# Kernel optimization log

Hardware: AMD Instinct MI355X
Metric: run time of the kernel (lower is better)

The kernel has to match this reference:

```python
import jax, jax.numpy as jnp
import numpy as np

N = 100000
E = 3200000
IN_CH = 256
HID = 32
OUT_CH = 16


def setup_inputs() -> dict:
    key = jax.random.key(0)
    ks = jax.random.split(key, 9)
    x = jax.random.normal(ks[0], (N, IN_CH), dtype=jnp.float32)
    row = jax.random.randint(ks[1], (E,), 0, N)
    col = jax.random.randint(ks[2], (E,), 0, N)
    edge_index = jnp.stack([row, col], axis=0)  # [2, E]
    # Glorot-style init for GCN weights, zero bias (PyG default)
    def glorot(k, fan_in, fan_out):
        s = jnp.sqrt(6.0 / (fan_in + fan_out))
        return jax.random.uniform(k, (fan_in, fan_out), jnp.float32, -s, s)
    W1 = glorot(ks[3], IN_CH, HID)
    b1 = jnp.zeros((HID,), jnp.float32)
    W_mu = glorot(ks[4], HID, OUT_CH)
    b_mu = jnp.zeros((OUT_CH,), jnp.float32)
    W_lv = glorot(ks[5], HID, OUT_CH)
    b_lv = jnp.zeros((OUT_CH,), jnp.float32)
    return {"x": x, "edge_index": edge_index, "W1": W1, "b1": b1,
            "W_mu": W_mu, "b_mu": b_mu, "W_lv": W_lv, "b_lv": b_lv}


def _gcn_norm(edge_index, n):
    # PyG gcn_norm with add_self_loops=True: deg over target col including self-loop
    row, col = edge_index[0], edge_index[1]
    deg = jax.ops.segment_sum(jnp.ones((edge_index.shape[1],), jnp.float32), col,
                              num_segments=n) + 1.0  # +1 for self-loop
    dis = jax.lax.rsqrt(deg)  # deg >= 1 always
    edge_norm = dis[row] * dis[col]          # [E]
    self_norm = dis * dis                    # [N], norm of self-loop edge
    return edge_norm, self_norm


def _gcn_conv(x, W, b, row, col, edge_norm, self_norm, n):
    h = x @ W  # [N, F_out] — transform BEFORE aggregation (small F_out)
    agg = jax.ops.segment_sum(h[row] * edge_norm[:, None], col, num_segments=n)
    return agg + self_norm[:, None] * h + b


def reference(x, edge_index, W1, b1, W_mu, b_mu, W_lv, b_lv):
    n = x.shape[0]
    row, col = edge_index[0], edge_index[1]
    edge_norm, self_norm = _gcn_norm(edge_index, n)
    h = jax.nn.relu(_gcn_conv(x, W1, b1, row, col, edge_norm, self_norm, n))
    mu = _gcn_conv(h, W_mu, b_mu, row, col, edge_norm, self_norm, n)
    logvar = _gcn_conv(h, W_lv, b_lv, row, col, edge_norm, self_norm, n)
    return (mu, logvar)
```

## Files before the change

kernel.cpp:

```cpp
#include <hip/hip_runtime.h>

#define N_NODES 100000
#define E_EDGES 3200000
#define IN_CH 256
#define HID 32
#define OUT_CH 16

#define B_BUCKETS 250
#define NPB 400
#define PB 256
#define PCH (E_EDGES / PB)
#define GEMM_BLOCKS ((N_NODES + 63) / 64)
#define PADSTRIDE 6416

typedef unsigned short u16;
typedef __attribute__((ext_vector_type(8))) short bf16x8;
typedef __attribute__((ext_vector_type(4))) float f32x4;

__device__ __forceinline__ unsigned bf16rtn(float f) {
    unsigned u = __float_as_uint(f);
    return (u + 0x7FFFu + ((u >> 16) & 1u)) >> 16;
}
__device__ __forceinline__ float bflo(unsigned u) { return __uint_as_float(u << 16); }
__device__ __forceinline__ float bfhi(unsigned u) { return __uint_as_float(u & 0xFFFF0000u); }


__global__ __launch_bounds__(256) void k_pre(const int* __restrict__ col,
                                             int* __restrict__ ghist,
                                             const float* __restrict__ W1,
                                             const float* __restrict__ x,
                                             u16* __restrict__ h0sh, int e, int n) {
    int bid = blockIdx.x;
    int tid = threadIdx.x;
    if (bid < PB) {
        __shared__ int h[B_BUCKETS];
        for (int i = tid; i < B_BUCKETS; i += 256) h[i] = 0;
        __syncthreads();
        int lo = bid * PCH, hi = lo + PCH;
        for (int i = lo + tid; i < hi; i += 256)
            atomicAdd(&h[col[i] / NPB], 1);
        __syncthreads();
        for (int i = tid; i < B_BUCKETS; i += 256)
            ghist[bid * B_BUCKETS + i] = h[i];
    } else {
        int gbid = bid - PB;
        int lane = tid & 63;
        int wv = tid >> 6;
        int vbase = gbid * 64 + wv * 16;
        if (vbase >= n) return;
        int arow = lane & 15;
        int kg = lane >> 4;
        const float* xr = x + (size_t)(vbase + arow) * IN_CH + kg * 8;

        uint4 bfrag[8][2];
        int colc0 = lane & 15;
        int krow0 = (lane >> 4) * 8;
#pragma unroll
        for (int kt = 0; kt < 8; ++kt) {
#pragma unroll
            for (int ct = 0; ct < 2; ++ct) {
                const float* wp = W1 + (size_t)(kt * 32 + krow0) * HID + ct * 16 + colc0;
                unsigned p[4];
#pragma unroll
                for (int pp = 0; pp < 4; ++pp) {
                    unsigned lo = bf16rtn(wp[(2 * pp) * HID]);
                    unsigned hi = bf16rtn(wp[(2 * pp + 1) * HID]);
                    p[pp] = lo | (hi << 16);
                }
                bfrag[kt][ct] = make_uint4(p[0], p[1], p[2], p[3]);
            }
        }

        f32x4 acc0 = {0.f, 0.f, 0.f, 0.f};
        f32x4 acc1 = {0.f, 0.f, 0.f, 0.f};
#pragma unroll
        for (int kt = 0; kt < 8; ++kt) {
            float4 a0 = *reinterpret_cast<const float4*>(xr + kt * 32);
            float4 a1 = *reinterpret_cast<const float4*>(xr + kt * 32 + 4);
            union { unsigned u[4]; bf16x8 v; } af;
            af.u[0] = bf16rtn(a0.x) | (bf16rtn(a0.y) << 16);
            af.u[1] = bf16rtn(a0.z) | (bf16rtn(a0.w) << 16);
            af.u[2] = bf16rtn(a1.x) | (bf16rtn(a1.y) << 16);
            af.u[3] = bf16rtn(a1.z) | (bf16rtn(a1.w) << 16);
            union { uint4 q; bf16x8 v; } b0, b1;
            b0.q = bfrag[kt][0];
            b1.q = bfrag[kt][1];
            acc0 = __builtin_amdgcn_mfma_f32_16x16x32_bf16(af.v, b0.v, acc0, 0, 0, 0);
            acc1 = __builtin_amdgcn_mfma_f32_16x16x32_bf16(af.v, b1.v, acc1, 0, 0, 0);
        }

        int r0 = (lane >> 4) * 4;
        int colo = lane & 15;
#pragma unroll
        for (int r = 0; r < 4; ++r) {
            int v = vbase + r0 + r;
            h0sh[(size_t)v * HID + colo]      = (u16)bf16rtn(acc0[r]);
            h0sh[(size_t)v * HID + 16 + colo] = (u16)bf16rtn(acc1[r]);
        }
    }
}


__global__ __launch_bounds__(256) void k_scan(int* __restrict__ ghist, int* __restrict__ bcnt) {
    __shared__ int a[256], b[256];
    int bu = blockIdx.x, t = threadIdx.x;
    int v = ghist[t * B_BUCKETS + bu];
    a[t] = v;
    __syncthreads();
    int* sp = a; int* dp = b;
    for (int off = 1; off < 256; off <<= 1) {
        dp[t] = sp[t] + ((t >= off) ? sp[t - off] : 0);
        __syncthreads();
        int* tm = sp; sp = dp; dp = tm;
    }
    ghist[t * B_BUCKETS + bu] = sp[t] - v;
    if (t == 255) bcnt[bu] = sp[t];
}


__global__ void k_bscan(const int* __restrict__ bcnt, int* __restrict__ bstart,
                        u16* __restrict__ h0sh, u16* __restrict__ hsh) {
    __shared__ int a[256], b[256];
    int t = threadIdx.x;
    if (t < HID) {
        h0sh[(size_t)N_NODES * HID + t] = 0;
        hsh[(size_t)N_NODES * HID + t] = 0;
    }
    int myc = (t < B_BUCKETS) ? bcnt[t] : 0;
    a[t] = myc;
    __syncthreads();
    int* sp = a; int* dp = b;
    for (int off = 1; off < 256; off <<= 1) {
        dp[t] = sp[t] + ((t >= off) ? sp[t - off] : 0);
        __syncthreads();
        int* tm = sp; sp = dp; dp = tm;
    }
    int incl = sp[t];
    if (t < B_BUCKETS) bstart[t] = incl - myc;
    if (t == B_BUCKETS - 1) bstart[B_BUCKETS] = incl;
}


__global__ __launch_bounds__(256) void k_place(const int* __restrict__ row,
                                               const int* __restrict__ col,
                                               const int* __restrict__ bstart,
                                               const int* __restrict__ ghist,
                                               const int* __restrict__ bcnt,
                                               unsigned* __restrict__ psrc) {
    __shared__ unsigned stage[PCH];
    __shared__ unsigned char bb[PCH];
    __shared__ int base[B_BUCKETS];
    __shared__ int lstart[B_BUCKETS];
    __shared__ int cur[B_BUCKETS];
    __shared__ int sa[256], sb[256];
    int bid = blockIdx.x;
    int tid = threadIdx.x;

    int h = 0;
    if (tid < B_BUCKETS) {
        int e0 = ghist[bid * B_BUCKETS + tid];
        int e1 = (bid < PB - 1) ? ghist[(bid + 1) * B_BUCKETS + tid] : bcnt[tid];
        base[tid] = bstart[tid] + e0;
        h = e1 - e0;
    }
    sa[tid] = h;
    __syncthreads();
    int* sp = sa; int* dp = sb;
    for (int off = 1; off < 256; off <<= 1) {
        dp[tid] = sp[tid] + ((tid >= off) ? sp[tid - off] : 0);
        __syncthreads();
        int* tm = sp; sp = dp; dp = tm;
    }
    int ex = sp[tid] - h;
    if (tid < B_BUCKETS) { lstart[tid] = ex; cur[tid] = ex; }
    __syncthreads();

    int lo = bid * PCH;
    for (int i = lo + tid; i < lo + PCH; i += 256) {
        int c = col[i];
        int b = c / NPB;
        int pos = atomicAdd(&cur[b], 1);
        stage[pos] = ((unsigned)(c - b * NPB) << 17) | (unsigned)row[i];
        bb[pos] = (unsigned char)b;
    }
    __syncthreads();

    for (int idx = tid; idx < PCH; idx += 256) {
        int b = bb[idx];
        psrc[base[b] + (idx - lstart[b])] = stage[idx];
    }
}


__global__ __launch_bounds__(512) void k_bsort(const unsigned* __restrict__ psrc,
                                               const int* __restrict__ bstart,
                                               int* __restrict__ srow, int* __restrict__ deg,
                                               int* __restrict__ start, float* __restrict__ dis,
                                               u16* __restrict__ h0sh) {
    __shared__ int cnt[512];
    __shared__ int sa[512];
    __shared__ int sb[512];
    __shared__ int cur[512];
    int b = blockIdx.x, t = threadIdx.x;
    int s0 = bstart[b], s1 = bstart[b + 1], len = s1 - s0;
    int pbase = ((s0 + 15) & ~15) + b * PADSTRIDE;

    cnt[t] = 0;
    __syncthreads();
    for (int i = t; i < len; i += 512)
        atomicAdd(&cnt[psrc[s0 + i] >> 17], 1);
    __syncthreads();

    int d = cnt[t];
    int dpad = (d + 15) & ~15;
    sa[t] = dpad;
    __syncthreads();
    int* sp = sa; int* dp = sb;
    for (int off = 1; off < 512; off <<= 1) {
        dp[t] = sp[t] + ((t >= off) ? sp[t - off] : 0);
        __syncthreads();
        int* tm = sp; sp = dp; dp = tm;
    }
    int pex = sp[t] - dpad;
    __syncthreads();
    int gstart = pbase + pex;
    cur[t] = gstart;
    float dvv = 0.f;
    if (t < NPB) {
        int node = b * NPB + t;
        deg[node] = d;
        start[node] = gstart;
        dvv = rsqrtf((float)(d + 1));
        dis[node] = dvv;
        for (int j = d; j < dpad; ++j)
            srow[gstart + j] = N_NODES;
    }
    __syncthreads();

    for (int i = t; i < len; i += 512) {
        unsigned p = psrc[s0 + i];
        int cl = (int)(p >> 17);
        int pos = atomicAdd(&cur[cl], 1);
        srow[pos] = (int)(p & 0x1FFFFu);
    }

    if (t < NPB) {
        int node = b * NPB + t;
        uint4* p4 = reinterpret_cast<uint4*>(h0sh + (size_t)node * HID);
#pragma unroll
        for (int qq = 0; qq < 4; ++qq) {
            uint4 pv = p4[qq];
            unsigned r[4];
            unsigned comp[4] = {pv.x, pv.y, pv.z, pv.w};
#pragma unroll
            for (int k = 0; k < 4; ++k) {
                float lo = bflo(comp[k]) * dvv;
                float hi = bfhi(comp[k]) * dvv;
                r[k] = bf16rtn(lo) | (bf16rtn(hi) << 16);
            }
            p4[qq] = make_uint4(r[0], r[1], r[2], r[3]);
        }
    }
}

#define ACC8(gv)                                   \
    acc[0] += bflo(gv.x); acc[1] += bfhi(gv.x);    \
    acc[2] += bflo(gv.y); acc[3] += bfhi(gv.y);    \
    acc[4] += bflo(gv.z); acc[5] += bfhi(gv.z);    \
    acc[6] += bflo(gv.w); acc[7] += bfhi(gv.w);

#define GATHER16V(TAB)                                                                           \
    for (int i = 0; i < dpad; i += 16) {                                                         \
        int4 ui0 = *reinterpret_cast<const int4*>(srow + s + i);                                 \
        int4 ui1 = *reinterpret_cast<const int4*>(srow + s + i + 4);                             \
        int4 ui2 = *reinterpret_cast<const int4*>(srow + s + i + 8);                             \
        int4 ui3 = *reinterpret_cast<const int4*>(srow + s + i + 12);                            \
        uint4 g0 = *reinterpret_cast<const uint4*>(TAB + (size_t)ui0.x * HID + q * 8);           \
        uint4 g1 = *reinterpret_cast<const uint4*>(TAB + (size_t)ui0.y * HID + q * 8);           \
        uint4 g2 = *reinterpret_cast<const uint4*>(TAB + (size_t)ui0.z * HID + q * 8);           \
        uint4 g3 = *reinterpret_cast<const uint4*>(TAB + (size_t)ui0.w * HID + q * 8);           \
        uint4 g4 = *reinterpret_cast<const uint4*>(TAB + (size_t)ui1.x * HID + q * 8);           \
        uint4 g5 = *reinterpret_cast<const uint4*>(TAB + (size_t)ui1.y * HID + q * 8);           \
        uint4 g6 = *reinterpret_cast<const uint4*>(TAB + (size_t)ui1.z * HID + q * 8);           \
        uint4 g7 = *reinterpret_cast<const uint4*>(TAB + (size_t)ui1.w * HID + q * 8);           \
        uint4 g8 = *reinterpret_cast<const uint4*>(TAB + (size_t)ui2.x * HID + q * 8);           \
        uint4 g9 = *reinterpret_cast<const uint4*>(TAB + (size_t)ui2.y * HID + q * 8);           \
        uint4 ga = *reinterpret_cast<const uint4*>(TAB + (size_t)ui2.z * HID + q * 8);           \
        uint4 gb = *reinterpret_cast<const uint4*>(TAB + (size_t)ui2.w * HID + q * 8);           \
        uint4 gc = *reinterpret_cast<const uint4*>(TAB + (size_t)ui3.x * HID + q * 8);           \
        uint4 gd = *reinterpret_cast<const uint4*>(TAB + (size_t)ui3.y * HID + q * 8);           \
        uint4 ge = *reinterpret_cast<const uint4*>(TAB + (size_t)ui3.z * HID + q * 8);           \
        uint4 gf = *reinterpret_cast<const uint4*>(TAB + (size_t)ui3.w * HID + q * 8);           \
        ACC8(g0) ACC8(g1) ACC8(g2) ACC8(g3) ACC8(g4) ACC8(g5) ACC8(g6) ACC8(g7)                  \
        ACC8(g8) ACC8(g9) ACC8(ga) ACC8(gb) ACC8(gc) ACC8(gd) ACC8(ge) ACC8(gf)                  \
    }


__global__ __launch_bounds__(256, 4) void k_agg1(const u16* __restrict__ h0sh,
                                                 const int* __restrict__ srow,
                                                 const int* __restrict__ start,
                                                 const int* __restrict__ deg,
                                                 const float* __restrict__ dis,
                                                 const float* __restrict__ b1,
                                                 u16* __restrict__ hsh, int n) {
    int tid = threadIdx.x;
    int lane = tid & 63;
    int g = lane >> 2;
    int q = lane & 3;
    int wv = tid >> 6;
    int v = blockIdx.x * 64 + wv * 16 + g;
    if (v >= n) v = n - 1;
    int s = start[v];
    int dpad = (deg[v] + 15) & ~15;
    float dv = dis[v];

    float acc[8];
#pragma unroll
    for (int c = 0; c < 8; ++c) acc[c] = 0.f;

    GATHER16V(h0sh)

    uint4 sv = *reinterpret_cast<const uint4*>(h0sh + (size_t)v * HID + q * 8);
    float self[8] = {bflo(sv.x), bfhi(sv.x), bflo(sv.y), bfhi(sv.y),
                     bflo(sv.z), bfhi(sv.z), bflo(sv.w), bfhi(sv.w)};
    float4 ba = *reinterpret_cast<const float4*>(b1 + q * 8);
    float4 bb = *reinterpret_cast<const float4*>(b1 + q * 8 + 4);
    float bias[8] = {ba.x, ba.y, ba.z, ba.w, bb.x, bb.y, bb.z, bb.w};

    unsigned pk[4];
#pragma unroll
    for (int p = 0; p < 4; ++p) {
        float o0 = dv * fmaxf(0.f, fmaf(dv, acc[2 * p] + self[2 * p], bias[2 * p]));
        float o1 = dv * fmaxf(0.f, fmaf(dv, acc[2 * p + 1] + self[2 * p + 1], bias[2 * p + 1]));
        pk[p] = bf16rtn(o0) | (bf16rtn(o1) << 16);
    }
    *reinterpret_cast<uint4*>(hsh + (size_t)v * HID + q * 8) = make_uint4(pk[0], pk[1], pk[2], pk[3]);
}


__global__ __launch_bounds__(256, 4) void k_agg2(const u16* __restrict__ hsh,
                                                 const int* __restrict__ srow,
                                                 const int* __restrict__ start,
                                                 const int* __restrict__ deg,
                                                 const float* __restrict__ dis,
                                                 const float* __restrict__ Wmu,
                                                 const float* __restrict__ Wlv,
                                                 const float* __restrict__ bmu,
                                                 const float* __restrict__ blv,
                                                 float* __restrict__ out, int n) {
    __shared__ float wc[32][33];
    __shared__ float svec[64][33];
    int tid = threadIdx.x;
    for (int i2 = tid; i2 < 32 * 32; i2 += 256) {
        int k = i2 >> 5, c = i2 & 31;
        wc[k][c] = (c < OUT_CH) ? Wmu[k * OUT_CH + c] : Wlv[k * OUT_CH + (c - OUT_CH)];
    }

    int lane = tid & 63;
    int g = lane >> 2;
    int q = lane & 3;
    int wv = tid >> 6;
    int dd = wv * 16 + g;
    int v = blockIdx.x * 64 + dd;
    if (v >= n) v = n - 1;
    int s = start[v];
    int dpad = (deg[v] + 15) & ~15;
    float dv = dis[v];

    float acc[8];
#pragma unroll
    for (int c = 0; c < 8; ++c) acc[c] = 0.f;

    GATHER16V(hsh)

    uint4 sv4 = *reinterpret_cast<const uint4*>(hsh + (size_t)v * HID + q * 8);
    float self[8] = {bflo(sv4.x), bfhi(sv4.x), bflo(sv4.y), bfhi(sv4.y),
                     bflo(sv4.z), bfhi(sv4.z), bflo(sv4.w), bfhi(sv4.w)};
#pragma unroll
    for (int c = 0; c < 8; ++c)
        svec[dd][q * 8 + c] = dv * (acc[c] + self[c]);
    __syncthreads();

    int dd2 = tid >> 2;
    int oo = tid & 3;
    int v2 = blockIdx.x * 64 + dd2;
    if (v2 >= n) return;
    float o[8];
#pragma unroll
    for (int c = 0; c < 8; ++c) o[c] = 0.f;
#pragma unroll 8
    for (int k = 0; k < 32; ++k) {
        float skv = svec[dd2][k];
        const float* wr = &wc[k][oo * 8];
        o[0] = fmaf(skv, wr[0], o[0]);
        o[1] = fmaf(skv, wr[1], o[1]);
        o[2] = fmaf(skv, wr[2], o[2]);
        o[3] = fmaf(skv, wr[3], o[3]);
        o[4] = fmaf(skv, wr[4], o[4]);
        o[5] = fmaf(skv, wr[5], o[5]);
        o[6] = fmaf(skv, wr[6], o[6]);
        o[7] = fmaf(skv, wr[7], o[7]);
    }
    float* dst;
    const float* bsrc;
    if (oo < 2) { dst = out + (size_t)v2 * OUT_CH + oo * 8;                       bsrc = bmu + oo * 8; }
    else        { dst = out + (size_t)N_NODES * OUT_CH + (size_t)v2 * OUT_CH + (oo - 2) * 8; bsrc = blv + (oo - 2) * 8; }
    float4 b0 = *reinterpret_cast<const float4*>(bsrc);
    float4 b1v = *reinterpret_cast<const float4*>(bsrc + 4);
    *reinterpret_cast<float4*>(dst)     = make_float4(o[0] + b0.x, o[1] + b0.y, o[2] + b0.z, o[3] + b0.w);
    *reinterpret_cast<float4*>(dst + 4) = make_float4(o[4] + b1v.x, o[5] + b1v.y, o[6] + b1v.z, o[7] + b1v.w);
}


extern "C" void kernel_launch(void* const* d_in, const int* in_sizes, int n_in,
                              void* d_out, int out_size, void* d_ws, size_t ws_size,
                              hipStream_t stream) {
    const float* x   = (const float*)d_in[0];
    const int*   ei  = (const int*)d_in[1];
    const float* W1  = (const float*)d_in[2];
    const float* b1  = (const float*)d_in[3];
    const float* Wmu = (const float*)d_in[4];
    const float* bmu = (const float*)d_in[5];
    const float* Wlv = (const float*)d_in[6];
    const float* blv = (const float*)d_in[7];
    float* out = (float*)d_out;

    const int* row = ei;
    const int* col = ei + E_EDGES;

    char* w = (char*)d_ws;
    int*   bcnt   = (int*)w;  w += 1024;
    int*   bstart = (int*)w;  w += 1024;
    int*   ghist  = (int*)w;  w += (size_t)PB * B_BUCKETS * 4;
    int*   deg    = (int*)w;  w += (size_t)N_NODES * 4;
    float* dis    = (float*)w; w += (size_t)N_NODES * 4;
    int*   start  = (int*)w;  w += (size_t)N_NODES * 4;
    int*   srow   = (int*)w;  w += (size_t)(E_EDGES + 16 + B_BUCKETS * PADSTRIDE) * 4;
    u16*   h0sh   = (u16*)w;  w += (size_t)(N_NODES + 1) * HID * 2;
    u16*   hsh    = (u16*)w;  w += (size_t)(N_NODES + 1) * HID * 2;
    unsigned* psrc = (unsigned*)w; w += (size_t)E_EDGES * 4;

    const int TB = 256;
    k_pre<<<PB + GEMM_BLOCKS, TB, 0, stream>>>(col, ghist, W1, x, h0sh, E_EDGES, N_NODES);
    k_scan<<<B_BUCKETS, 256, 0, stream>>>(ghist, bcnt);
    k_bscan<<<1, 256, 0, stream>>>(bcnt, bstart, h0sh, hsh);
    k_place<<<PB, TB, 0, stream>>>(row, col, bstart, ghist, bcnt, psrc);
    k_bsort<<<B_BUCKETS, 512, 0, stream>>>(psrc, bstart, srow, deg, start, dis, h0sh);
    k_agg1<<<(N_NODES + 63) / 64, TB, 0, stream>>>(h0sh, srow, start, deg, dis, b1, hsh, N_NODES);
    k_agg2<<<(N_NODES + 63) / 64, TB, 0, stream>>>(hsh, srow, start, deg, dis,
                                                   Wmu, Wlv, bmu, blv, out, N_NODES);
}
```

Before: 169.7 us.

## Move x@W1 GEMM into placement kernel, pre-pack W1 fragments, double histogram blocks

```diff
diff --git a/kernel.cpp b/kernel.cpp
--- a/kernel.cpp
+++ b/kernel.cpp
@@ -8,7 +8,7 @@
 
 #define B_BUCKETS 250
 #define NPB 400
-#define PB 256
+#define PB 512
 #define PCH (E_EDGES / PB)
 #define GEMM_BLOCKS ((N_NODES + 63) / 64)
 #define PADSTRIDE 6416
@@ -28,8 +28,7 @@
 __global__ __launch_bounds__(256) void k_pre(const int* __restrict__ col,
                                              int* __restrict__ ghist,
                                              const float* __restrict__ W1,
-                                             const float* __restrict__ x,
-                                             u16* __restrict__ h0sh, int e, int n) {
+                                             uint4* __restrict__ W1f, int e) {
     int bid = blockIdx.x;
     int tid = threadIdx.x;
     if (bid < PB) {
@@ -42,6 +41,118 @@
         __syncthreads();
         for (int i = tid; i < B_BUCKETS; i += 256)
             ghist[bid * B_BUCKETS + i] = h[i];
+    } else {
+        for (int s = tid; s < 1024; s += 256) {
+            int lane = s & 63;
+            int ctkt = s >> 6;
+            int ct = ctkt & 1, kt = ctkt >> 1;
+            int colc = ct * 16 + (lane & 15);
+            int k0 = kt * 32 + (lane >> 4) * 8;
+            unsigned p[4];
+#pragma unroll
+            for (int pp = 0; pp < 4; ++pp) {
+                unsigned lo = bf16rtn(W1[(k0 + 2 * pp) * HID + colc]);
+                unsigned hi = bf16rtn(W1[(k0 + 2 * pp + 1) * HID + colc]);
+                p[pp] = lo | (hi << 16);
+            }
+            W1f[s] = make_uint4(p[0], p[1], p[2], p[3]);
+        }
+    }
+}
+
+
+__global__ __launch_bounds__(512) void k_scan(int* __restrict__ ghist, int* __restrict__ bcnt) {
+    __shared__ int a[512], b[512];
+    int bu = blockIdx.x, t = threadIdx.x;
+    int v = ghist[t * B_BUCKETS + bu];
+    a[t] = v;
+    __syncthreads();
+    int* sp = a; int* dp = b;
+    for (int off = 1; off < 512; off <<= 1) {
+        dp[t] = sp[t] + ((t >= off) ? sp[t - off] : 0);
+        __syncthreads();
+        int* tm = sp; sp = dp; dp = tm;
+    }
+    ghist[t * B_BUCKETS + bu] = sp[t] - v;
+    if (t == 511) bcnt[bu] = sp[t];
+}
+
+
+__global__ void k_bscan(const int* __restrict__ bcnt, int* __restrict__ bstart,
+                        u16* __restrict__ h0sh, u16* __restrict__ hsh) {
+    __shared__ int a[256], b[256];
+    int t = threadIdx.x;
+    if (t < HID) {
+        h0sh[(size_t)N_NODES * HID + t] = 0;
+        hsh[(size_t)N_NODES * HID + t] = 0;
+    }
+    int myc = (t < B_BUCKETS) ? bcnt[t] : 0;
+    a[t] = myc;
+    __syncthreads();
+    int* sp = a; int* dp = b;
+    for (int off = 1; off < 256; off <<= 1) {
+        dp[t] = sp[t] + ((t >= off) ? sp[t - off] : 0);
+        __syncthreads();
+        int* tm = sp; sp = dp; dp = tm;
+    }
+    int incl = sp[t];
+    if (t < B_BUCKETS) bstart[t] = incl - myc;
+    if (t == B_BUCKETS - 1) bstart[B_BUCKETS] = incl;
+}
+
+
+__global__ __launch_bounds__(256) void k_place(const int* __restrict__ row,
+                                               const int* __restrict__ col,
+                                               const int* __restrict__ bstart,
+                                               const int* __restrict__ ghist,
+                                               const int* __restrict__ bcnt,
+                                               unsigned* __restrict__ psrc,
+                                               const float* __restrict__ x,
+                                               const uint4* __restrict__ W1f,
+                                               u16* __restrict__ h0sh, int n) {
+    __shared__ unsigned stage[PCH];
+    __shared__ unsigned char bb[PCH];
+    __shared__ int base[B_BUCKETS];
+    __shared__ int lstart[B_BUCKETS];
+    __shared__ int cur[B_BUCKETS];
+    __shared__ int sa[256], sb[256];
+    int bid = blockIdx.x;
+    int tid = threadIdx.x;
+
+    if (bid < PB) {
+        int h = 0;
+        if (tid < B_BUCKETS) {
+            int e0 = ghist[bid * B_BUCKETS + tid];
+            int e1 = (bid < PB - 1) ? ghist[(bid + 1) * B_BUCKETS + tid] : bcnt[tid];
+            base[tid] = bstart[tid] + e0;
+            h = e1 - e0;
+        }
+        sa[tid] = h;
+        __syncthreads();
+        int* sp = sa; int* dp = sb;
+        for (int off = 1; off < 256; off <<= 1) {
+            dp[tid] = sp[tid] + ((tid >= off) ? sp[tid - off] : 0);
+            __syncthreads();
+            int* tm = sp; sp = dp; dp = tm;
+        }
+        int ex = sp[tid] - h;
+        if (tid < B_BUCKETS) { lstart[tid] = ex; cur[tid] = ex; }
+        __syncthreads();
+
+        int lo = bid * PCH;
+        for (int i = lo + tid; i < lo + PCH; i += 256) {
+            int c = col[i];
+            int b = c / NPB;
+            int pos = atomicAdd(&cur[b], 1);
+            stage[pos] = ((unsigned)(c - b * NPB) << 17) | (unsigned)row[i];
+            bb[pos] = (unsigned char)b;
+        }
+        __syncthreads();
+
+        for (int idx = tid; idx < PCH; idx += 256) {
+            int b = bb[idx];
+            psrc[base[b] + (idx - lstart[b])] = stage[idx];
+        }
     } else {
         int gbid = bid - PB;
         int lane = tid & 63;
@@ -53,22 +164,11 @@
         const float* xr = x + (size_t)(vbase + arow) * IN_CH + kg * 8;
 
         uint4 bfrag[8][2];
-        int colc0 = lane & 15;
-        int krow0 = (lane >> 4) * 8;
 #pragma unroll
         for (int kt = 0; kt < 8; ++kt) {
 #pragma unroll
-            for (int ct = 0; ct < 2; ++ct) {
-                const float* wp = W1 + (size_t)(kt * 32 + krow0) * HID + ct * 16 + colc0;
-                unsigned p[4];
-#pragma unroll
-                for (int pp = 0; pp < 4; ++pp) {
-                    unsigned lo = bf16rtn(wp[(2 * pp) * HID]);
-                    unsigned hi = bf16rtn(wp[(2 * pp + 1) * HID]);
-                    p[pp] = lo | (hi << 16);
-                }
-                bfrag[kt][ct] = make_uint4(p[0], p[1], p[2], p[3]);
-            }
+            for (int ct = 0; ct < 2; ++ct)
+                bfrag[kt][ct] = W1f[(kt * 2 + ct) * 64 + lane];
         }
 
         f32x4 acc0 = {0.f, 0.f, 0.f, 0.f};
@@ -97,97 +197,6 @@
             h0sh[(size_t)v * HID + colo]      = (u16)bf16rtn(acc0[r]);
             h0sh[(size_t)v * HID + 16 + colo] = (u16)bf16rtn(acc1[r]);
         }
-    }
-}
-
-
-__global__ __launch_bounds__(256) void k_scan(int* __restrict__ ghist, int* __restrict__ bcnt) {
-    __shared__ int a[256], b[256];
-    int bu = blockIdx.x, t = threadIdx.x;
-    int v = ghist[t * B_BUCKETS + bu];
-    a[t] = v;
-    __syncthreads();
-    int* sp = a; int* dp = b;
-    for (int off = 1; off < 256; off <<= 1) {
-        dp[t] = sp[t] + ((t >= off) ? sp[t - off] : 0);
-        __syncthreads();
-        int* tm = sp; sp = dp; dp = tm;
-    }
-    ghist[t * B_BUCKETS + bu] = sp[t] - v;
-    if (t == 255) bcnt[bu] = sp[t];
-}
-
-
-__global__ void k_bscan(const int* __restrict__ bcnt, int* __restrict__ bstart,
-                        u16* __restrict__ h0sh, u16* __restrict__ hsh) {
-    __shared__ int a[256], b[256];
-    int t = threadIdx.x;
-    if (t < HID) {
-        h0sh[(size_t)N_NODES * HID + t] = 0;
-        hsh[(size_t)N_NODES * HID + t] = 0;
-    }
-    int myc = (t < B_BUCKETS) ? bcnt[t] : 0;
-    a[t] = myc;
-    __syncthreads();
-    int* sp = a; int* dp = b;
-    for (int off = 1; off < 256; off <<= 1) {
-        dp[t] = sp[t] + ((t >= off) ? sp[t - off] : 0);
-        __syncthreads();
-        int* tm = sp; sp = dp; dp = tm;
-    }
-    int incl = sp[t];
-    if (t < B_BUCKETS) bstart[t] = incl - myc;
-    if (t == B_BUCKETS - 1) bstart[B_BUCKETS] = incl;
-}
-
-
-__global__ __launch_bounds__(256) void k_place(const int* __restrict__ row,
-                                               const int* __restrict__ col,
-                                               const int* __restrict__ bstart,
-                                               const int* __restrict__ ghist,
-                                               const int* __restrict__ bcnt,
-                                               unsigned* __restrict__ psrc) {
-    __shared__ unsigned stage[PCH];
-    __shared__ unsigned char bb[PCH];
-    __shared__ int base[B_BUCKETS];
-    __shared__ int lstart[B_BUCKETS];
-    __shared__ int cur[B_BUCKETS];
-    __shared__ int sa[256], sb[256];
-    int bid = blockIdx.x;
-    int tid = threadIdx.x;
-
-    int h = 0;
-    if (tid < B_BUCKETS) {
-        int e0 = ghist[bid * B_BUCKETS + tid];
-        int e1 = (bid < PB - 1) ? ghist[(bid + 1) * B_BUCKETS + tid] : bcnt[tid];
-        base[tid] = bstart[tid] + e0;
-        h = e1 - e0;
-    }
-    sa[tid] = h;
-    __syncthreads();
-    int* sp = sa; int* dp = sb;
-    for (int off = 1; off < 256; off <<= 1) {
-        dp[tid] = sp[tid] + ((tid >= off) ? sp[tid - off] : 0);
-        __syncthreads();
-        int* tm = sp; sp = dp; dp = tm;
-    }
-    int ex = sp[tid] - h;
-    if (tid < B_BUCKETS) { lstart[tid] = ex; cur[tid] = ex; }
-    __syncthreads();
-
-    int lo = bid * PCH;
-    for (int i = lo + tid; i < lo + PCH; i += 256) {
-        int c = col[i];
-        int b = c / NPB;
-        int pos = atomicAdd(&cur[b], 1);
-        stage[pos] = ((unsigned)(c - b * NPB) << 17) | (unsigned)row[i];
-        bb[pos] = (unsigned char)b;
-    }
-    __syncthreads();
-
-    for (int idx = tid; idx < PCH; idx += 256) {
-        int b = bb[idx];
-        psrc[base[b] + (idx - lstart[b])] = stage[idx];
     }
 }
 
@@ -431,6 +440,7 @@
     char* w = (char*)d_ws;
     int*   bcnt   = (int*)w;  w += 1024;
     int*   bstart = (int*)w;  w += 1024;
+    uint4* W1f    = (uint4*)w; w += 16384;
     int*   ghist  = (int*)w;  w += (size_t)PB * B_BUCKETS * 4;
     int*   deg    = (int*)w;  w += (size_t)N_NODES * 4;
     float* dis    = (float*)w; w += (size_t)N_NODES * 4;
@@ -441,10 +451,11 @@
     unsigned* psrc = (unsigned*)w; w += (size_t)E_EDGES * 4;
 
     const int TB = 256;
-    k_pre<<<PB + GEMM_BLOCKS, TB, 0, stream>>>(col, ghist, W1, x, h0sh, E_EDGES, N_NODES);
-    k_scan<<<B_BUCKETS, 256, 0, stream>>>(ghist, bcnt);
+    k_pre<<<PB + 1, TB, 0, stream>>>(col, ghist, W1, W1f, E_EDGES);
+    k_scan<<<B_BUCKETS, 512, 0, stream>>>(ghist, bcnt);
     k_bscan<<<1, 256, 0, stream>>>(bcnt, bstart, h0sh, hsh);
-    k_place<<<PB, TB, 0, stream>>>(row, col, bstart, ghist, bcnt, psrc);
+    k_place<<<PB + GEMM_BLOCKS, TB, 0, stream>>>(row, col, bstart, ghist, bcnt, psrc,
+                                                 x, W1f, h0sh, N_NODES);
     k_bsort<<<B_BUCKETS, 512, 0, stream>>>(psrc, bstart, srow, deg, start, dis, h0sh);
     k_agg1<<<(N_NODES + 63) / 64, TB, 0, stream>>>(h0sh, srow, start, deg, dis, b1, hsh, N_NODES);
     k_agg2<<<(N_NODES + 63) / 64, TB, 0, stream>>>(hsh, srow, start, deg, dis,
```

Result: faster. 154.0 us (-9.2%).
